# Kernel optimization log

Measured on AMD Instinct MI355X. Metric: run time of the kernel, lower is better.

The kernel has to match this reference:

```python
import jax, jax.numpy as jnp
import numpy as np

N_NODES = 50000
N_EDGES = 800000
N_FEAT = 128
N_HID = 128
N_LAYER = 4
N_CLASS = 40


def setup_inputs() -> dict:
    key = jax.random.key(0)
    ks = jax.random.split(key, 8)
    x = jax.random.normal(ks[0], (N_NODES, N_FEAT), jnp.float32)
    edge_index = jax.random.randint(ks[1], (2, N_EDGES), 0, N_NODES, dtype=jnp.int64)
    s = 1.0 / np.float32(np.sqrt(N_HID))
    # n_feat == n_hid so all L conv weights stack into one [L, C, C] tensor
    convW = jax.random.normal(ks[2], (N_LAYER, N_HID, N_HID), jnp.float32) * s
    convb = jnp.zeros((N_LAYER, N_HID), jnp.float32)
    W_att = jax.random.normal(ks[3], (N_HID, N_HID), jnp.float32) * s
    a_att = jax.random.normal(ks[4], (N_HID,), jnp.float32) * s
    W_out = jax.random.normal(ks[5], (N_HID, N_CLASS), jnp.float32) * s
    b_out = jnp.zeros((N_CLASS,), jnp.float32)
    return dict(x=x, edge_index=edge_index, convW=convW, convb=convb,
                W_att=W_att, a_att=a_att, W_out=W_out, b_out=b_out)


def reference(x, edge_index, convW, convb, W_att, a_att, W_out, b_out):
    src, dst = edge_index[0], edge_index[1]
    N = x.shape[0]
    # GCN symmetric normalization with self-loops: deg = 1 + in-degree
    deg = jax.ops.segment_sum(jnp.ones_like(dst, dtype=jnp.float32), dst,
                              num_segments=N) + 1.0
    dinv = jax.lax.rsqrt(deg)
    enorm = (dinv[src] * dinv[dst])[:, None]   # per-edge norm
    snorm = (dinv * dinv)[:, None]             # self-loop norm

    hs = []
    h = x
    for l in range(N_LAYER):
        hW = h @ convW[l]                                          # [N, C]
        agg = jax.ops.segment_sum(hW[src] * enorm, dst, num_segments=N)
        agg = agg + hW * snorm                                     # self-loop
        h = jax.nn.relu(agg + convb[l])
        # dropout is identity at inference (training=False)
        hs.append(h)

    H = jnp.stack(hs, axis=1)                                      # [N, L, C]
    # additive attention over layers: alpha_l = softmax_l(a . tanh(W h_l))
    scores = jnp.tanh(H @ W_att) @ a_att                           # [N, L]
    alpha = jax.nn.softmax(scores, axis=1)
    fused = jnp.einsum('nl,nlc->nc', alpha, H)                     # [N, C]
    return fused @ W_out + b_out                                   # [N, n_class]
```

## Files before the change

kernel.cpp:

```cpp
#include <hip/hip_runtime.h>

#define NNODES 50000
#define NEDGES 800000
#define NCLASS 40
#define NBLK_SCAN 196
#define CNTB  3125
#define PREPB 320
#define WOUTB 24
#define GEMMB 782
#define XBLK  3125

typedef _Float16 half8  __attribute__((ext_vector_type(8)));
typedef float    floatx4 __attribute__((ext_vector_type(4)));

#define CSTR 136
#define SMEM_BYTES (64 * CSTR * 2 + 256)

__device__ __forceinline__ float fast_tanh(float x) {
    return 1.0f - 2.0f / (__expf(2.0f * x) + 1.0f);
}

__global__ __launch_bounds__(256) void k_pre(const int* __restrict__ dst, int* __restrict__ cnt,
                                             int* __restrict__ rank,
                                             const float* __restrict__ convW, const float* __restrict__ W_att,
                                             _Float16* __restrict__ WT,
                                             const float* __restrict__ Wout, _Float16* __restrict__ WoutT) {
    int bid = blockIdx.x, tid = threadIdx.x;
    if (bid < CNTB) {
        int e = bid * 256 + tid;
        rank[e] = atomicAdd(&cnt[dst[e]], 1);
    } else if (bid < CNTB + PREPB) {
        int idx = (bid - CNTB) * 256 + tid;
        int mat = idx >> 14, rem = idx & 16383;
        int j = rem & 7, lane = (rem >> 3) & 63, tile = rem >> 9;
        int l15 = lane & 15, quad = lane >> 4;
        int ct = tile & 7, kk = tile >> 3;
        int n = ct * 16 + l15, k = kk * 32 + quad * 8 + j;
        const float* src = (mat < 4) ? (convW + mat * 16384) : W_att;
        WT[idx] = (_Float16)src[k * 128 + n];
    } else {
        int idx = (bid - CNTB - PREPB) * 256 + tid;
        int j = idx & 7, lane = (idx >> 3) & 63, tile = idx >> 9;
        int l15 = lane & 15, quad = lane >> 4;
        int ct = tile % 3, kk = tile / 3;
        int n = ct * 16 + l15, k = kk * 32 + quad * 8 + j;
        WoutT[idx] = (n < NCLASS) ? (_Float16)Wout[k * NCLASS + n] : (_Float16)0.f;
    }
}

__global__ __launch_bounds__(256) void k_bsum(const int* __restrict__ cnt, int* __restrict__ bsum) {
    int t = threadIdx.x, b = blockIdx.x;
    int i = b * 256 + t;
    int c = (i < NNODES) ? cnt[i] : 0;
    int v = c;
    v += __shfl_xor(v, 1);  v += __shfl_xor(v, 2);  v += __shfl_xor(v, 4);
    v += __shfl_xor(v, 8);  v += __shfl_xor(v, 16); v += __shfl_xor(v, 32);
    __shared__ int ws[4];
    if ((t & 63) == 0) ws[t >> 6] = v;
    __syncthreads();
    if (t == 0) bsum[b] = ws[0] + ws[1] + ws[2] + ws[3];
}

__global__ __launch_bounds__(256) void k_offsets(const int* __restrict__ cnt, const int* __restrict__ bsum,
                                                 int* __restrict__ offsets, float* __restrict__ dinv) {
    int t = threadIdx.x, b = blockIdx.x;
    int i = b * 256 + t;
    int c = (i < NNODES) ? cnt[i] : 0;
    int pv = (t < b) ? bsum[t] : 0;
    int rv = pv;
    rv += __shfl_xor(rv, 1);  rv += __shfl_xor(rv, 2);  rv += __shfl_xor(rv, 4);
    rv += __shfl_xor(rv, 8);  rv += __shfl_xor(rv, 16); rv += __shfl_xor(rv, 32);
    __shared__ int wsum[4];
    __shared__ int part[256];
    if ((t & 63) == 0) wsum[t >> 6] = rv;
    part[t] = c;
    __syncthreads();
    int boff = wsum[0] + wsum[1] + wsum[2] + wsum[3];
#pragma unroll
    for (int d = 1; d < 256; d <<= 1) {
        int v = (t >= d) ? part[t - d] : 0;
        __syncthreads();
        part[t] += v;
        __syncthreads();
    }
    if (i < NNODES) {
        offsets[i] = boff + part[t] - c;
        dinv[i] = rsqrtf((float)c + 1.0f);
    }
    if (b == 0 && t == 0) offsets[NNODES] = NEDGES;
}

__device__ __forceinline__ void gemm_body_f32(const float* __restrict__ Av, const _Float16* __restrict__ WTf,
                                              const float* __restrict__ dinv, _Float16* __restrict__ C,
                                              int m0, char* smem) {
    _Float16 (*Csh)[CSTR] = (_Float16 (*)[CSTR])smem;
    float* sdinv = (float*)(smem + 64 * CSTR * 2);
    int tid = threadIdx.x;
    int wave = tid >> 6, lane = tid & 63;
    int quad = lane >> 4, l15 = lane & 15;
    int ko = quad * 8;

    if (tid < 64) {
        int r = m0 + tid; if (r > NNODES - 1) r = NNODES - 1;
        sdinv[tid] = dinv[r];
    }

    floatx4 acc[4][2];
#pragma unroll
    for (int rt = 0; rt < 4; ++rt)
#pragma unroll
        for (int ct = 0; ct < 2; ++ct) acc[rt][ct] = (floatx4){0.f, 0.f, 0.f, 0.f};

#pragma unroll
    for (int kk = 0; kk < 4; ++kk) {
        half8 a[4], b[2];
#pragma unroll
        for (int rt = 0; rt < 4; ++rt) {
            int row = m0 + rt * 16 + l15;
            if (row > NNODES - 1) row = NNODES - 1;
            const float* Ap = Av + (size_t)row * 128 + kk * 32 + ko;
            float4 f0 = *(const float4*)Ap;
            float4 f1 = *(const float4*)(Ap + 4);
            a[rt] = (half8){(_Float16)f0.x, (_Float16)f0.y, (_Float16)f0.z, (_Float16)f0.w,
                            (_Float16)f1.x, (_Float16)f1.y, (_Float16)f1.z, (_Float16)f1.w};
        }
#pragma unroll
        for (int ct = 0; ct < 2; ++ct)
            b[ct] = *(const half8*)&WTf[((kk * 8 + (wave * 2 + ct)) * 64 + lane) * 8];
#pragma unroll
        for (int rt = 0; rt < 4; ++rt)
#pragma unroll
            for (int ct = 0; ct < 2; ++ct)
                acc[rt][ct] = __builtin_amdgcn_mfma_f32_16x16x32_f16(a[rt], b[ct], acc[rt][ct], 0, 0, 0);
    }
    __syncthreads();

#pragma unroll
    for (int rt = 0; rt < 4; ++rt)
#pragma unroll
        for (int r = 0; r < 4; ++r) {
            float d = sdinv[rt * 16 + quad * 4 + r];
#pragma unroll
            for (int ct = 0; ct < 2; ++ct)
                Csh[rt * 16 + quad * 4 + r][wave * 32 + ct * 16 + l15] = (_Float16)(acc[rt][ct][r] * d);
        }
    __syncthreads();

    int row = tid >> 2, seg = tid & 3;
    int gm = m0 + row;
    if (gm < NNODES) {
#pragma unroll
        for (int j = 0; j < 4; ++j)
            *(half8*)(C + (size_t)gm * 128 + seg * 32 + j * 8) = *(const half8*)&Csh[row][seg * 32 + j * 8];
    }
}

__global__ __launch_bounds__(256) void k_fillgemm(const int* __restrict__ src, const int* __restrict__ dst,
                                                  const int* __restrict__ offsets, const int* __restrict__ rank,
                                                  int* __restrict__ esrc,
                                                  const float* __restrict__ x, const _Float16* __restrict__ WT,
                                                  const float* __restrict__ dinv, _Float16* __restrict__ C) {
    __shared__ __align__(16) char smem[SMEM_BYTES];
    int bid = blockIdx.x;
    if (bid < GEMMB) {
        gemm_body_f32(x, WT, dinv, C, bid * 64, smem);
    } else {
        int e = (bid - GEMMB) * 256 + threadIdx.x;
        int d = dst[e];
        esrc[offsets[d] + rank[e]] = src[e];
    }
}

template <bool HAS_GEMM>
__global__ __launch_bounds__(256) void k_layer(const _Float16* __restrict__ hin,
                                               const int* __restrict__ offsets, const int* __restrict__ esrc,
                                               const float* __restrict__ dinv, const float* __restrict__ bias,
                                               _Float16* __restrict__ hh,
                                               const _Float16* __restrict__ WTatt, const float* __restrict__ a_att,
                                               float* __restrict__ scores, int layer,
                                               const _Float16* __restrict__ WTnext, _Float16* __restrict__ hout) {
    __shared__ __align__(16) _Float16 h[16][CSTR];
    __shared__ float bsh[128];
    __shared__ float sdv[16];
    __shared__ float pp[4][16];
    int tid = threadIdx.x;
    if (tid < 128) bsh[tid] = bias[tid];
    int wave = tid >> 6, lane = tid & 63;
    int n0 = blockIdx.x * 16;

    {
        int nl = tid >> 4;
        int cl = tid & 15;
        int c8 = cl * 8;
        int n = n0 + nl;
        int beg = offsets[n], end = offsets[n + 1];
        float dn = dinv[n];
        half8 sv = *(const half8*)(hin + (size_t)n * 128 + c8);

        float a[8];
#pragma unroll
        for (int u = 0; u < 8; ++u) a[u] = 0.f;

        int i0[4], i1[4];
#pragma unroll
        for (int i = 0; i < 4; ++i) {
            int ei = beg + i;
            int t = esrc[ei];
            i0[i] = (ei < end) ? t : NNODES;
        }
        half8 v0[4];
#pragma unroll
        for (int i = 0; i < 4; ++i) v0[i] = *(const half8*)(hin + (size_t)i0[i] * 128 + c8);
#pragma unroll
        for (int i = 0; i < 4; ++i) {
            int ei = beg + 4 + i;
            int t = esrc[ei];
            i1[i] = (ei < end) ? t : NNODES;
        }
        half8 v1[4];
#pragma unroll
        for (int i = 0; i < 4; ++i) v1[i] = *(const half8*)(hin + (size_t)i1[i] * 128 + c8);

        for (int e = beg; e < end; e += 8) {
            int i2[4];
#pragma unroll
            for (int i = 0; i < 4; ++i) {
                int ei = e + 8 + i;
                int t = esrc[ei];
                i2[i] = (ei < end) ? t : NNODES;
            }
#pragma unroll
            for (int i = 0; i < 4; ++i)
#pragma unroll
                for (int u = 0; u < 8; ++u) a[u] += (float)v0[i][u];
#pragma unroll
            for (int i = 0; i < 4; ++i) v0[i] = *(const half8*)(hin + (size_t)i2[i] * 128 + c8);
            int i3[4];
#pragma unroll
            for (int i = 0; i < 4; ++i) {
                int ei = e + 12 + i;
                int t = esrc[ei];
                i3[i] = (ei < end) ? t : NNODES;
            }
#pragma unroll
            for (int i = 0; i < 4; ++i)
#pragma unroll
                for (int u = 0; u < 8; ++u) a[u] += (float)v1[i][u];
#pragma unroll
            for (int i = 0; i < 4; ++i) v1[i] = *(const half8*)(hin + (size_t)i3[i] * 128 + c8);
        }
        __syncthreads();
        half8 o;
#pragma unroll
        for (int u = 0; u < 8; ++u) {
            float r = (a[u] + (float)sv[u]) * dn + bsh[c8 + u];
            o[u] = (_Float16)fmaxf(r, 0.f);
        }
        *(half8*)(hh + (size_t)n * 128 + c8) = o;
        *(half8*)&h[nl][c8] = o;
        if (cl == 0) sdv[nl] = dn;
    }
    __syncthreads();

    int quad = lane >> 4, l15 = lane & 15;
    int ko = quad * 8;
    half8 af[4];
#pragma unroll
    for (int kk = 0; kk < 4; ++kk) af[kk] = *(const half8*)&h[l15][kk * 32 + ko];

    {
        float p[4] = {0.f, 0.f, 0.f, 0.f};
#pragma unroll
        for (int c2 = 0; c2 < 2; ++c2) {
            int ct = wave * 2 + c2;
            half8 b[4];
#pragma unroll
            for (int kk = 0; kk < 4; ++kk)
                b[kk] = *(const half8*)&WTatt[((kk * 8 + ct) * 64 + lane) * 8];
            floatx4 acc = (floatx4){0.f, 0.f, 0.f, 0.f};
#pragma unroll
            for (int kk = 0; kk < 4; ++kk)
                acc = __builtin_amdgcn_mfma_f32_16x16x32_f16(af[kk], b[kk], acc, 0, 0, 0);
            float av = a_att[ct * 16 + l15];
#pragma unroll
            for (int r = 0; r < 4; ++r) p[r] += av * fast_tanh(acc[r]);
        }
#pragma unroll
        for (int r = 0; r < 4; ++r) {
            float v = p[r];
            v += __shfl_xor(v, 1); v += __shfl_xor(v, 2);
            v += __shfl_xor(v, 4); v += __shfl_xor(v, 8);
            if (l15 == 0) pp[wave][quad * 4 + r] = v;
        }
    }
    __syncthreads();
    if (tid < 16) scores[(size_t)(n0 + tid) * 4 + layer] = pp[0][tid] + pp[1][tid] + pp[2][tid] + pp[3][tid];

    if (HAS_GEMM) {
        floatx4 acc[2];
#pragma unroll
        for (int c2 = 0; c2 < 2; ++c2) acc[c2] = (floatx4){0.f, 0.f, 0.f, 0.f};
#pragma unroll
        for (int c2 = 0; c2 < 2; ++c2) {
            int ct = wave * 2 + c2;
#pragma unroll
            for (int kk = 0; kk < 4; ++kk) {
                half8 b = *(const half8*)&WTnext[((kk * 8 + ct) * 64 + lane) * 8];
                acc[c2] = __builtin_amdgcn_mfma_f32_16x16x32_f16(af[kk], b, acc[c2], 0, 0, 0);
            }
        }
        __syncthreads();
#pragma unroll
        for (int c2 = 0; c2 < 2; ++c2) {
            int col = (wave * 2 + c2) * 16 + l15;
#pragma unroll
            for (int r = 0; r < 4; ++r) {
                int row = quad * 4 + r;
                h[row][col] = (_Float16)(acc[c2][r] * sdv[row]);
            }
        }
        __syncthreads();
        int row = tid >> 4, seg = tid & 15;
        int gm = n0 + row;
        *(half8*)(hout + (size_t)gm * 128 + seg * 8) = *(const half8*)&h[row][seg * 8];
    }
}

__global__ __launch_bounds__(256) void k_fuse_out(const _Float16* __restrict__ hbase, const float* __restrict__ scores,
                                                  const _Float16* __restrict__ WoutT, const float* __restrict__ bout,
                                                  float* __restrict__ out) {
    __shared__ __align__(16) _Float16 Fs[64][136];
    __shared__ float salpha[256];
    const size_t LSTR = (size_t)NNODES * 128;
    int tid = threadIdx.x;
    int n0 = blockIdx.x * 64;

    if (tid < 64) {
        int node = n0 + tid; if (node > NNODES - 1) node = NNODES - 1;
        float4 s = *(const float4*)(scores + (size_t)node * 4);
        float mx = fmaxf(fmaxf(s.x, s.y), fmaxf(s.z, s.w));
        float e0 = __expf(s.x - mx), e1 = __expf(s.y - mx), e2 = __expf(s.z - mx), e3 = __expf(s.w - mx);
        float inv = 1.0f / (e0 + e1 + e2 + e3);
        salpha[tid * 4 + 0] = e0 * inv; salpha[tid * 4 + 1] = e1 * inv;
        salpha[tid * 4 + 2] = e2 * inv; salpha[tid * 4 + 3] = e3 * inv;
    }
    __syncthreads();

    {
        int no = tid >> 2, seg = tid & 3;
        int node = n0 + no; if (node > NNODES - 1) node = NNODES - 1;
        float al0 = salpha[no * 4 + 0], al1 = salpha[no * 4 + 1];
        float al2 = salpha[no * 4 + 2], al3 = salpha[no * 4 + 3];
        const _Float16* hp = hbase + (size_t)node * 128 + seg * 32;
#pragma unroll
        for (int j = 0; j < 4; ++j) {
            half8 h0 = *(const half8*)(hp + 0 * LSTR + j * 8);
            half8 h1 = *(const half8*)(hp + 1 * LSTR + j * 8);
            half8 h2 = *(const half8*)(hp + 2 * LSTR + j * 8);
            half8 h3 = *(const half8*)(hp + 3 * LSTR + j * 8);
            half8 f;
#pragma unroll
            for (int u = 0; u < 8; ++u)
                f[u] = (_Float16)(al0 * (float)h0[u] + al1 * (float)h1[u] +
                                  al2 * (float)h2[u] + al3 * (float)h3[u]);
            *(half8*)&Fs[no][seg * 32 + j * 8] = f;
        }
    }
    __syncthreads();

    int wave = tid >> 6, lane = tid & 63;
    int quad = lane >> 4, l15 = lane & 15;
    int ko = quad * 8;
    half8 ff[4];
    int frow = wave * 16 + l15;
#pragma unroll
    for (int kk = 0; kk < 4; ++kk) ff[kk] = *(const half8*)&Fs[frow][kk * 32 + ko];
#pragma unroll
    for (int ct = 0; ct < 3; ++ct) {
        half8 bw[4];
#pragma unroll
        for (int kk = 0; kk < 4; ++kk)
            bw[kk] = *(const half8*)(WoutT + ((kk * 3 + ct) * 64 + lane) * 8);
        floatx4 acc = (floatx4){0.f, 0.f, 0.f, 0.f};
#pragma unroll
        for (int kk = 0; kk < 4; ++kk)
            acc = __builtin_amdgcn_mfma_f32_16x16x32_f16(ff[kk], bw[kk], acc, 0, 0, 0);
        int col = ct * 16 + l15;
        if (col < NCLASS) {
            float bv = bout[col];
#pragma unroll
            for (int r = 0; r < 4; ++r) {
                int node = n0 + wave * 16 + quad * 4 + r;
                if (node < NNODES) out[(size_t)node * NCLASS + col] = acc[r] + bv;
            }
        }
    }
}

extern "C" void kernel_launch(void* const* d_in, const int* in_sizes, int n_in,
                              void* d_out, int out_size, void* d_ws, size_t ws_size,
                              hipStream_t stream) {
    const float* x     = (const float*)d_in[0];
    const int*   ei    = (const int*)d_in[1];
    const float* convW = (const float*)d_in[2];
    const float* convb = (const float*)d_in[3];
    const float* W_att = (const float*)d_in[4];
    const float* a_att = (const float*)d_in[5];
    const float* W_out = (const float*)d_in[6];
    const float* b_out = (const float*)d_in[7];
    float* out = (float*)d_out;

    char* ws = (char*)d_ws;
    size_t off = 0;
    auto take = [&](size_t nbytes) { char* p = ws + off; off += (nbytes + 255) & ~(size_t)255; return p; };
    float*     dinv    = (float*)take(NNODES * 4);
    int*       cnt     = (int*)take(NNODES * 4);
    int*       rank    = (int*)take(NEDGES * 4);
    int*       offsets = (int*)take((NNODES + 1) * 4);
    int*       bsum    = (int*)take(256 * 4);
    int*       esrc    = (int*)take(NEDGES * 4 + 256);
    _Float16*  WoutT   = (_Float16*)take((size_t)48 * 128 * 2);
    float*     scores  = (float*)take(NNODES * 4 * 4);
    _Float16*  WT      = (_Float16*)take((size_t)5 * 128 * 128 * 2);
    _Float16*  hWsA    = (_Float16*)take((size_t)(NNODES + 1) * 128 * 2);
    _Float16*  hh[4];
    for (int l = 0; l < 4; ++l) hh[l] = (_Float16*)take((size_t)NNODES * 128 * 2);
    _Float16*  hWsB    = (_Float16*)take((size_t)(NNODES + 1) * 128 * 2);

    const int* src = ei;
    const int* dst = ei + NEDGES;

    hipMemsetAsync(cnt, 0, NNODES * 4, stream);
    hipMemsetAsync(hWsA + (size_t)NNODES * 128, 0, 256, stream);
    hipMemsetAsync(hWsB + (size_t)NNODES * 128, 0, 256, stream);
    k_pre<<<CNTB + PREPB + WOUTB, 256, 0, stream>>>(dst, cnt, rank, convW, W_att, WT, W_out, WoutT);
    k_bsum<<<NBLK_SCAN, 256, 0, stream>>>(cnt, bsum);
    k_offsets<<<NBLK_SCAN, 256, 0, stream>>>(cnt, bsum, offsets, dinv);
    k_fillgemm<<<GEMMB + CNTB, 256, 0, stream>>>(src, dst, offsets, rank, esrc, x, WT, dinv, hWsA);

    k_layer<true><<<XBLK, 256, 0, stream>>>(hWsA, offsets, esrc, dinv, convb + 0 * 128, hh[0],
                                            WT + 4 * 16384, a_att, scores, 0, WT + 1 * 16384, hWsB);
    k_layer<true><<<XBLK, 256, 0, stream>>>(hWsB, offsets, esrc, dinv, convb + 1 * 128, hh[1],
                                            WT + 4 * 16384, a_att, scores, 1, WT + 2 * 16384, hWsA);
    k_layer<true><<<XBLK, 256, 0, stream>>>(hWsA, offsets, esrc, dinv, convb + 2 * 128, hh[2],
                                            WT + 4 * 16384, a_att, scores, 2, WT + 3 * 16384, hWsB);
    k_layer<false><<<XBLK, 256, 0, stream>>>(hWsB, offsets, esrc, dinv, convb + 3 * 128, hh[3],
                                             WT + 4 * 16384, a_att, scores, 3, (const _Float16*)nullptr,
                                             (_Float16*)nullptr);
    k_fuse_out<<<GEMMB, 256, 0, stream>>>(hh[0], scores, WoutT, b_out, out);
}
```

Baseline: 330.3 us.

## Split layer into channel-blocked gather kernel and separate attention/GEMM kernel

Transformed features are stored in four 32-channel column blocks so that each aggregation block gathers only one 64-byte slice per neighbor, which keeps the gathered working set small enough to stay cache-resident. The fused per-layer kernel is split into a gather/aggregation kernel and a 64-row MFMA kernel for the attention score and next-layer GEMM. This adds a write and re-read of hh per layer plus an extra launch per layer. It also replaces the padding memsets with a block in the prep kernel.

```diff
diff --git a/kernel.cpp b/kernel.cpp
--- a/kernel.cpp
+++ b/kernel.cpp
@@ -8,13 +8,15 @@
 #define PREPB 320
 #define WOUTB 24
 #define GEMMB 782
-#define XBLK  3125
+#define AGGT  782
+#define AGGB  (AGGT * 4)
 
 typedef _Float16 half8  __attribute__((ext_vector_type(8)));
 typedef float    floatx4 __attribute__((ext_vector_type(4)));
 
 #define CSTR 136
-#define SMEM_BYTES (64 * CSTR * 2 + 256)
+#define BLKROW 32
+#define BLKSTRIDE ((size_t)(NNODES + 1) * BLKROW)
 
 __device__ __forceinline__ float fast_tanh(float x) {
     return 1.0f - 2.0f / (__expf(2.0f * x) + 1.0f);
@@ -24,7 +26,8 @@
                                              int* __restrict__ rank,
                                              const float* __restrict__ convW, const float* __restrict__ W_att,
                                              _Float16* __restrict__ WT,
-                                             const float* __restrict__ Wout, _Float16* __restrict__ WoutT) {
+                                             const float* __restrict__ Wout, _Float16* __restrict__ WoutT,
+                                             _Float16* __restrict__ blkA, _Float16* __restrict__ blkB) {
     int bid = blockIdx.x, tid = threadIdx.x;
     if (bid < CNTB) {
         int e = bid * 256 + tid;
@@ -38,13 +41,18 @@
         int n = ct * 16 + l15, k = kk * 32 + quad * 8 + j;
         const float* src = (mat < 4) ? (convW + mat * 16384) : W_att;
         WT[idx] = (_Float16)src[k * 128 + n];
-    } else {
+    } else if (bid < CNTB + PREPB + WOUTB) {
         int idx = (bid - CNTB - PREPB) * 256 + tid;
         int j = idx & 7, lane = (idx >> 3) & 63, tile = idx >> 9;
         int l15 = lane & 15, quad = lane >> 4;
         int ct = tile % 3, kk = tile / 3;
         int n = ct * 16 + l15, k = kk * 32 + quad * 8 + j;
         WoutT[idx] = (n < NCLASS) ? (_Float16)Wout[k * NCLASS + n] : (_Float16)0.f;
+    } else {
+        int s = tid >> 7, rem = tid & 127;
+        int cg = rem >> 5, c = rem & 31;
+        _Float16* p = (s == 0) ? blkA : blkB;
+        p[(size_t)cg * BLKSTRIDE + (size_t)NNODES * BLKROW + c] = (_Float16)0.f;
     }
 }
 
@@ -91,7 +99,7 @@
 }
 
 __device__ __forceinline__ void gemm_body_f32(const float* __restrict__ Av, const _Float16* __restrict__ WTf,
-                                              const float* __restrict__ dinv, _Float16* __restrict__ C,
+                                              const float* __restrict__ dinv, _Float16* __restrict__ Cblk,
                                               int m0, char* smem) {
     _Float16 (*Csh)[CSTR] = (_Float16 (*)[CSTR])smem;
     float* sdinv = (float*)(smem + 64 * CSTR * 2);
@@ -151,7 +159,8 @@
     if (gm < NNODES) {
 #pragma unroll
         for (int j = 0; j < 4; ++j)
-            *(half8*)(C + (size_t)gm * 128 + seg * 32 + j * 8) = *(const half8*)&Csh[row][seg * 32 + j * 8];
+            *(half8*)(Cblk + (size_t)seg * BLKSTRIDE + (size_t)gm * BLKROW + j * 8) =
+                *(const half8*)&Csh[row][seg * 32 + j * 8];
     }
 }
 
@@ -159,11 +168,11 @@
                                                   const int* __restrict__ offsets, const int* __restrict__ rank,
                                                   int* __restrict__ esrc,
                                                   const float* __restrict__ x, const _Float16* __restrict__ WT,
-                                                  const float* __restrict__ dinv, _Float16* __restrict__ C) {
-    __shared__ __align__(16) char smem[SMEM_BYTES];
+                                                  const float* __restrict__ dinv, _Float16* __restrict__ Cblk) {
+    __shared__ __align__(16) char smem[64 * CSTR * 2 + 256];
     int bid = blockIdx.x;
     if (bid < GEMMB) {
-        gemm_body_f32(x, WT, dinv, C, bid * 64, smem);
+        gemm_body_f32(x, WT, dinv, Cblk, bid * 64, smem);
     } else {
         int e = (bid - GEMMB) * 256 + threadIdx.x;
         int d = dst[e];
@@ -171,105 +180,124 @@
     }
 }
 
+__global__ __launch_bounds__(256) void k_agg(const _Float16* __restrict__ hinblk,
+                                             const int* __restrict__ offsets, const int* __restrict__ esrc,
+                                             const float* __restrict__ dinv, const float* __restrict__ bias,
+                                             _Float16* __restrict__ hh) {
+    int tid = threadIdx.x;
+    int cg = blockIdx.x & 3, tile = blockIdx.x >> 2;
+    int nl = tid >> 2, cl = tid & 3;
+    int n = tile * 64 + nl;
+    if (n >= NNODES) return;
+    int c8 = cl * 8;
+    const _Float16* base = hinblk + (size_t)cg * BLKSTRIDE;
+    int beg = offsets[n], end = offsets[n + 1];
+    float dn = dinv[n];
+    half8 sv = *(const half8*)(base + (size_t)n * BLKROW + c8);
+    float4 b0 = *(const float4*)(bias + cg * 32 + c8);
+    float4 b1 = *(const float4*)(bias + cg * 32 + c8 + 4);
+
+    float a[8];
+#pragma unroll
+    for (int u = 0; u < 8; ++u) a[u] = 0.f;
+
+    int i0[4], i1[4];
+#pragma unroll
+    for (int i = 0; i < 4; ++i) {
+        int ei = beg + i;
+        int t = esrc[ei];
+        i0[i] = (ei < end) ? t : NNODES;
+    }
+    half8 v0[4];
+#pragma unroll
+    for (int i = 0; i < 4; ++i) v0[i] = *(const half8*)(base + (size_t)i0[i] * BLKROW + c8);
+#pragma unroll
+    for (int i = 0; i < 4; ++i) {
+        int ei = beg + 4 + i;
+        int t = esrc[ei];
+        i1[i] = (ei < end) ? t : NNODES;
+    }
+    half8 v1[4];
+#pragma unroll
+    for (int i = 0; i < 4; ++i) v1[i] = *(const half8*)(base + (size_t)i1[i] * BLKROW + c8);
+
+    for (int e = beg; e < end; e += 8) {
+        int i2[4];
+#pragma unroll
+        for (int i = 0; i < 4; ++i) {
+            int ei = e + 8 + i;
+            int t = esrc[ei];
+            i2[i] = (ei < end) ? t : NNODES;
+        }
+#pragma unroll
+        for (int i = 0; i < 4; ++i)
+#pragma unroll
+            for (int u = 0; u < 8; ++u) a[u] += (float)v0[i][u];
+#pragma unroll
+        for (int i = 0; i < 4; ++i) v0[i] = *(const half8*)(base + (size_t)i2[i] * BLKROW + c8);
+        int i3[4];
+#pragma unroll
+        for (int i = 0; i < 4; ++i) {
+            int ei = e + 12 + i;
+            int t = esrc[ei];
+            i3[i] = (ei < end) ? t : NNODES;
+        }
+#pragma unroll
+        for (int i = 0; i < 4; ++i)
+#pragma unroll
+            for (int u = 0; u < 8; ++u) a[u] += (float)v1[i][u];
+#pragma unroll
+        for (int i = 0; i < 4; ++i) v1[i] = *(const half8*)(base + (size_t)i3[i] * BLKROW + c8);
+    }
+
+    float bb[8] = {b0.x, b0.y, b0.z, b0.w, b1.x, b1.y, b1.z, b1.w};
+    half8 o;
+#pragma unroll
+    for (int u = 0; u < 8; ++u) {
+        float r = (a[u] + (float)sv[u]) * dn + bb[u];
+        o[u] = (_Float16)fmaxf(r, 0.f);
+    }
+    *(half8*)(hh + (size_t)n * 128 + cg * 32 + c8) = o;
+}
+
 template <bool HAS_GEMM>
-__global__ __launch_bounds__(256) void k_layer(const _Float16* __restrict__ hin,
-                                               const int* __restrict__ offsets, const int* __restrict__ esrc,
-                                               const float* __restrict__ dinv, const float* __restrict__ bias,
-                                               _Float16* __restrict__ hh,
-                                               const _Float16* __restrict__ WTatt, const float* __restrict__ a_att,
-                                               float* __restrict__ scores, int layer,
-                                               const _Float16* __restrict__ WTnext, _Float16* __restrict__ hout) {
-    __shared__ __align__(16) _Float16 h[16][CSTR];
-    __shared__ float bsh[128];
-    __shared__ float sdv[16];
-    __shared__ float pp[4][16];
+__global__ __launch_bounds__(256) void k_attngemm(const _Float16* __restrict__ hh,
+                                                  const float* __restrict__ dinv,
+                                                  const _Float16* __restrict__ WTatt,
+                                                  const float* __restrict__ a_att,
+                                                  float* __restrict__ scores, int layer,
+                                                  const _Float16* __restrict__ WTnext,
+                                                  _Float16* __restrict__ outblk) {
+    __shared__ __align__(16) _Float16 Csh[64][CSTR];
+    __shared__ float pp[4][64];
+    __shared__ float sdv[64];
     int tid = threadIdx.x;
-    if (tid < 128) bsh[tid] = bias[tid];
     int wave = tid >> 6, lane = tid & 63;
-    int n0 = blockIdx.x * 16;
-
-    {
-        int nl = tid >> 4;
-        int cl = tid & 15;
-        int c8 = cl * 8;
-        int n = n0 + nl;
-        int beg = offsets[n], end = offsets[n + 1];
-        float dn = dinv[n];
-        half8 sv = *(const half8*)(hin + (size_t)n * 128 + c8);
-
-        float a[8];
-#pragma unroll
-        for (int u = 0; u < 8; ++u) a[u] = 0.f;
-
-        int i0[4], i1[4];
-#pragma unroll
-        for (int i = 0; i < 4; ++i) {
-            int ei = beg + i;
-            int t = esrc[ei];
-            i0[i] = (ei < end) ? t : NNODES;
-        }
-        half8 v0[4];
-#pragma unroll
-        for (int i = 0; i < 4; ++i) v0[i] = *(const half8*)(hin + (size_t)i0[i] * 128 + c8);
-#pragma unroll
-        for (int i = 0; i < 4; ++i) {
-            int ei = beg + 4 + i;
-            int t = esrc[ei];
-            i1[i] = (ei < end) ? t : NNODES;
-        }
-        half8 v1[4];
-#pragma unroll
-        for (int i = 0; i < 4; ++i) v1[i] = *(const half8*)(hin + (size_t)i1[i] * 128 + c8);
-
-        for (int e = beg; e < end; e += 8) {
-            int i2[4];
-#pragma unroll
-            for (int i = 0; i < 4; ++i) {
-                int ei = e + 8 + i;
-                int t = esrc[ei];
-                i2[i] = (ei < end) ? t : NNODES;
-            }
-#pragma unroll
-            for (int i = 0; i < 4; ++i)
-#pragma unroll
-                for (int u = 0; u < 8; ++u) a[u] += (float)v0[i][u];
-#pragma unroll
-            for (int i = 0; i < 4; ++i) v0[i] = *(const half8*)(hin + (size_t)i2[i] * 128 + c8);
-            int i3[4];
-#pragma unroll
-            for (int i = 0; i < 4; ++i) {
-                int ei = e + 12 + i;
-                int t = esrc[ei];
-                i3[i] = (ei < end) ? t : NNODES;
-            }
-#pragma unroll
-            for (int i = 0; i < 4; ++i)
-#pragma unroll
-                for (int u = 0; u < 8; ++u) a[u] += (float)v1[i][u];
-#pragma unroll
-            for (int i = 0; i < 4; ++i) v1[i] = *(const half8*)(hin + (size_t)i3[i] * 128 + c8);
-        }
-        __syncthreads();
-        half8 o;
-#pragma unroll
-        for (int u = 0; u < 8; ++u) {
-            float r = (a[u] + (float)sv[u]) * dn + bsh[c8 + u];
-            o[u] = (_Float16)fmaxf(r, 0.f);
-        }
-        *(half8*)(hh + (size_t)n * 128 + c8) = o;
-        *(half8*)&h[nl][c8] = o;
-        if (cl == 0) sdv[nl] = dn;
-    }
-    __syncthreads();
-
     int quad = lane >> 4, l15 = lane & 15;
     int ko = quad * 8;
-    half8 af[4];
-#pragma unroll
-    for (int kk = 0; kk < 4; ++kk) af[kk] = *(const half8*)&h[l15][kk * 32 + ko];
+    int m0 = blockIdx.x * 64;
+
+    if (tid < 64) {
+        int r = m0 + tid; if (r > NNODES - 1) r = NNODES - 1;
+        sdv[tid] = dinv[r];
+    }
+
+    half8 a[4][4];
+#pragma unroll
+    for (int rt = 0; rt < 4; ++rt) {
+        int row = m0 + rt * 16 + l15;
+        if (row > NNODES - 1) row = NNODES - 1;
+        const _Float16* Ap = hh + (size_t)row * 128 + ko;
+#pragma unroll
+        for (int kk = 0; kk < 4; ++kk) a[rt][kk] = *(const half8*)(Ap + kk * 32);
+    }
 
     {
-        float p[4] = {0.f, 0.f, 0.f, 0.f};
+        float p[4][4];
+#pragma unroll
+        for (int rt = 0; rt < 4; ++rt)
+#pragma unroll
+            for (int r = 0; r < 4; ++r) p[rt][r] = 0.f;
 #pragma unroll
         for (int c2 = 0; c2 < 2; ++c2) {
             int ct = wave * 2 + c2;
@@ -277,52 +305,69 @@
 #pragma unroll
             for (int kk = 0; kk < 4; ++kk)
                 b[kk] = *(const half8*)&WTatt[((kk * 8 + ct) * 64 + lane) * 8];
-            floatx4 acc = (floatx4){0.f, 0.f, 0.f, 0.f};
-#pragma unroll
-            for (int kk = 0; kk < 4; ++kk)
-                acc = __builtin_amdgcn_mfma_f32_16x16x32_f16(af[kk], b[kk], acc, 0, 0, 0);
             float av = a_att[ct * 16 + l15];
 #pragma unroll
-            for (int r = 0; r < 4; ++r) p[r] += av * fast_tanh(acc[r]);
-        }
-#pragma unroll
-        for (int r = 0; r < 4; ++r) {
-            float v = p[r];
-            v += __shfl_xor(v, 1); v += __shfl_xor(v, 2);
-            v += __shfl_xor(v, 4); v += __shfl_xor(v, 8);
-            if (l15 == 0) pp[wave][quad * 4 + r] = v;
-        }
-    }
-    __syncthreads();
-    if (tid < 16) scores[(size_t)(n0 + tid) * 4 + layer] = pp[0][tid] + pp[1][tid] + pp[2][tid] + pp[3][tid];
+            for (int rt = 0; rt < 4; ++rt) {
+                floatx4 acc = (floatx4){0.f, 0.f, 0.f, 0.f};
+#pragma unroll
+                for (int kk = 0; kk < 4; ++kk)
+                    acc = __builtin_amdgcn_mfma_f32_16x16x32_f16(a[rt][kk], b[kk], acc, 0, 0, 0);
+#pragma unroll
+                for (int r = 0; r < 4; ++r) p[rt][r] += av * fast_tanh(acc[r]);
+            }
+        }
+#pragma unroll
+        for (int rt = 0; rt < 4; ++rt)
+#pragma unroll
+            for (int r = 0; r < 4; ++r) {
+                float v = p[rt][r];
+                v += __shfl_xor(v, 1); v += __shfl_xor(v, 2);
+                v += __shfl_xor(v, 4); v += __shfl_xor(v, 8);
+                if (l15 == 0) pp[wave][rt * 16 + quad * 4 + r] = v;
+            }
+    }
+    __syncthreads();
+    if (tid < 64) {
+        int nd = m0 + tid;
+        if (nd < NNODES) scores[(size_t)nd * 4 + layer] = pp[0][tid] + pp[1][tid] + pp[2][tid] + pp[3][tid];
+    }
 
     if (HAS_GEMM) {
-        floatx4 acc[2];
-#pragma unroll
-        for (int c2 = 0; c2 < 2; ++c2) acc[c2] = (floatx4){0.f, 0.f, 0.f, 0.f};
+        floatx4 acc[4][2];
+#pragma unroll
+        for (int rt = 0; rt < 4; ++rt)
+#pragma unroll
+            for (int c2 = 0; c2 < 2; ++c2) acc[rt][c2] = (floatx4){0.f, 0.f, 0.f, 0.f};
 #pragma unroll
         for (int c2 = 0; c2 < 2; ++c2) {
             int ct = wave * 2 + c2;
 #pragma unroll
             for (int kk = 0; kk < 4; ++kk) {
                 half8 b = *(const half8*)&WTnext[((kk * 8 + ct) * 64 + lane) * 8];
-                acc[c2] = __builtin_amdgcn_mfma_f32_16x16x32_f16(af[kk], b, acc[c2], 0, 0, 0);
+#pragma unroll
+                for (int rt = 0; rt < 4; ++rt)
+                    acc[rt][c2] = __builtin_amdgcn_mfma_f32_16x16x32_f16(a[rt][kk], b, acc[rt][c2], 0, 0, 0);
             }
         }
+#pragma unroll
+        for (int rt = 0; rt < 4; ++rt)
+#pragma unroll
+            for (int r = 0; r < 4; ++r) {
+                int row = rt * 16 + quad * 4 + r;
+                float d = sdv[row];
+#pragma unroll
+                for (int c2 = 0; c2 < 2; ++c2)
+                    Csh[row][(wave * 2 + c2) * 16 + l15] = (_Float16)(acc[rt][c2][r] * d);
+            }
         __syncthreads();
-#pragma unroll
-        for (int c2 = 0; c2 < 2; ++c2) {
-            int col = (wave * 2 + c2) * 16 + l15;
-#pragma unroll
-            for (int r = 0; r < 4; ++r) {
-                int row = quad * 4 + r;
-                h[row][col] = (_Float16)(acc[c2][r] * sdv[row]);
-            }
-        }
-        __syncthreads();
-        int row = tid >> 4, seg = tid & 15;
-        int gm = n0 + row;
-        *(half8*)(hout + (size_t)gm * 128 + seg * 8) = *(const half8*)&h[row][seg * 8];
+        int row = tid >> 2, seg = tid & 3;
+        int gm = m0 + row;
+        if (gm < NNODES) {
+#pragma unroll
+            for (int j = 0; j < 4; ++j)
+                *(half8*)(outblk + (size_t)seg * BLKSTRIDE + (size_t)gm * BLKROW + j * 8) =
+                    *(const half8*)&Csh[row][seg * 32 + j * 8];
+        }
     }
 }
 
@@ -422,30 +467,32 @@
     _Float16*  WoutT   = (_Float16*)take((size_t)48 * 128 * 2);
     float*     scores  = (float*)take(NNODES * 4 * 4);
     _Float16*  WT      = (_Float16*)take((size_t)5 * 128 * 128 * 2);
-    _Float16*  hWsA    = (_Float16*)take((size_t)(NNODES + 1) * 128 * 2);
+    _Float16*  blkA    = (_Float16*)take(4 * BLKSTRIDE * 2);
     _Float16*  hh[4];
     for (int l = 0; l < 4; ++l) hh[l] = (_Float16*)take((size_t)NNODES * 128 * 2);
-    _Float16*  hWsB    = (_Float16*)take((size_t)(NNODES + 1) * 128 * 2);
+    _Float16*  blkB    = (_Float16*)take(4 * BLKSTRIDE * 2);
 
     const int* src = ei;
     const int* dst = ei + NEDGES;
 
     hipMemsetAsync(cnt, 0, NNODES * 4, stream);
-    hipMemsetAsync(hWsA + (size_t)NNODES * 128, 0, 256, stream);
-    hipMemsetAsync(hWsB + (size_t)NNODES * 128, 0, 256, stream);
-    k_pre<<<CNTB + PREPB + WOUTB, 256, 0, stream>>>(dst, cnt, rank, convW, W_att, WT, W_out, WoutT);
+    k_pre<<<CNTB + PREPB + WOUTB + 1, 256, 0, stream>>>(dst, cnt, rank, convW, W_att, WT, W_out, WoutT,
+                                                        blkA, blkB);
     k_bsum<<<NBLK_SCAN, 256, 0, stream>>>(cnt, bsum);
     k_offsets<<<NBLK_SCAN, 256, 0, stream>>>(cnt, bsum, offsets, dinv);
-    k_fillgemm<<<GEMMB + CNTB, 256, 0, stream>>>(src, dst, offsets, rank, esrc, x, WT, dinv, hWsA);
-
-    k_layer<true><<<XBLK, 256, 0, stream>>>(hWsA, offsets, esrc, dinv, convb + 0 * 128, hh[0],
-                                            WT + 4 * 16384, a_att, scores, 0, WT + 1 * 16384, hWsB);
-    k_layer<true><<<XBLK, 256, 0, stream>>>(hWsB, offsets, esrc, dinv, convb + 1 * 128, hh[1],
-                                            WT + 4 * 16384, a_att, scores, 1, WT + 2 * 16384, hWsA);
-    k_layer<true><<<XBLK, 256, 0, stream>>>(hWsA, offsets, esrc, dinv, convb + 2 * 128, hh[2],
-                                            WT + 4 * 16384, a_att, scores, 2, WT + 3 * 16384, hWsB);
-    k_layer<false><<<XBLK, 256, 0, stream>>>(hWsB, offsets, esrc, dinv, convb + 3 * 128, hh[3],
-                                             WT + 4 * 16384, a_att, scores, 3, (const _Float16*)nullptr,
-                                             (_Float16*)nullptr);
+    k_fillgemm<<<GEMMB + CNTB, 256, 0, stream>>>(src, dst, offsets, rank, esrc, x, WT, dinv, blkA);
+
+    _Float16* bin = blkA;
+    _Float16* bout_ = blkB;
+    for (int l = 0; l < 4; ++l) {
+        k_agg<<<AGGB, 256, 0, stream>>>(bin, offsets, esrc, dinv, convb + l * 128, hh[l]);
+        if (l < 3)
+            k_attngemm<true><<<GEMMB, 256, 0, stream>>>(hh[l], dinv, WT + 4 * 16384, a_att, scores, l,
+                                                        WT + (l + 1) * 16384, bout_);
+        else
+            k_attngemm<false><<<GEMMB, 256, 0, stream>>>(hh[3], dinv, WT + 4 * 16384, a_att, scores, 3,
+                                                         (const _Float16*)nullptr, (_Float16*)nullptr);
+        _Float16* t = bin; bin = bout_; bout_ = t;
+    }
     k_fuse_out<<<GEMMB, 256, 0, stream>>>(hh[0], scores, WoutT, b_out, out);
 }
```

New measurement: 364.8 us. +10.4%, slower.

## Store hW in column-blocked layout so gathers run four passes over 32-column slices

Applied to the files above, without the earlier changes.

The transformed features hW are now stored as four column blocks of 32 halves per node instead of 128-wide rows. The layer kernel gathers one 32-column block at a time, with four lanes each handling different edges, then reduces across lanes with shuffles. Each pass touches a quarter-size array, so the gather working set fits cache better. In exchange, esrc indices and offsets are read four times, there are shuffle reductions, and each gathered row is only 64 bytes. The sentinel zero rows are now cleared inside k_pre instead of by separate memsets.

```diff
diff --git a/kernel.cpp b/kernel.cpp
--- a/kernel.cpp
+++ b/kernel.cpp
@@ -14,7 +14,8 @@
 typedef float    floatx4 __attribute__((ext_vector_type(4)));
 
 #define CSTR 136
-#define SMEM_BYTES (64 * CSTR * 2 + 256)
+#define BLKROW 32
+#define BLKSTRIDE ((size_t)(NNODES + 1) * BLKROW)
 
 __device__ __forceinline__ float fast_tanh(float x) {
     return 1.0f - 2.0f / (__expf(2.0f * x) + 1.0f);
@@ -24,7 +25,8 @@
                                              int* __restrict__ rank,
                                              const float* __restrict__ convW, const float* __restrict__ W_att,
                                              _Float16* __restrict__ WT,
-                                             const float* __restrict__ Wout, _Float16* __restrict__ WoutT) {
+                                             const float* __restrict__ Wout, _Float16* __restrict__ WoutT,
+                                             _Float16* __restrict__ blkA, _Float16* __restrict__ blkB) {
     int bid = blockIdx.x, tid = threadIdx.x;
     if (bid < CNTB) {
         int e = bid * 256 + tid;
@@ -38,13 +40,18 @@
         int n = ct * 16 + l15, k = kk * 32 + quad * 8 + j;
         const float* src = (mat < 4) ? (convW + mat * 16384) : W_att;
         WT[idx] = (_Float16)src[k * 128 + n];
-    } else {
+    } else if (bid < CNTB + PREPB + WOUTB) {
         int idx = (bid - CNTB - PREPB) * 256 + tid;
         int j = idx & 7, lane = (idx >> 3) & 63, tile = idx >> 9;
         int l15 = lane & 15, quad = lane >> 4;
         int ct = tile % 3, kk = tile / 3;
         int n = ct * 16 + l15, k = kk * 32 + quad * 8 + j;
         WoutT[idx] = (n < NCLASS) ? (_Float16)Wout[k * NCLASS + n] : (_Float16)0.f;
+    } else {
+        int s = tid >> 7, rem = tid & 127;
+        int cg = rem >> 5, c = rem & 31;
+        _Float16* p = (s == 0) ? blkA : blkB;
+        p[(size_t)cg * BLKSTRIDE + (size_t)NNODES * BLKROW + c] = (_Float16)0.f;
     }
 }
 
@@ -91,7 +98,7 @@
 }
 
 __device__ __forceinline__ void gemm_body_f32(const float* __restrict__ Av, const _Float16* __restrict__ WTf,
-                                              const float* __restrict__ dinv, _Float16* __restrict__ C,
+                                              const float* __restrict__ dinv, _Float16* __restrict__ Cblk,
                                               int m0, char* smem) {
     _Float16 (*Csh)[CSTR] = (_Float16 (*)[CSTR])smem;
     float* sdinv = (float*)(smem + 64 * CSTR * 2);
@@ -151,7 +158,8 @@
     if (gm < NNODES) {
 #pragma unroll
         for (int j = 0; j < 4; ++j)
-            *(half8*)(C + (size_t)gm * 128 + seg * 32 + j * 8) = *(const half8*)&Csh[row][seg * 32 + j * 8];
+            *(half8*)(Cblk + (size_t)seg * BLKSTRIDE + (size_t)gm * BLKROW + j * 8) =
+                *(const half8*)&Csh[row][seg * 32 + j * 8];
     }
 }
 
@@ -159,11 +167,11 @@
                                                   const int* __restrict__ offsets, const int* __restrict__ rank,
                                                   int* __restrict__ esrc,
                                                   const float* __restrict__ x, const _Float16* __restrict__ WT,
-                                                  const float* __restrict__ dinv, _Float16* __restrict__ C) {
-    __shared__ __align__(16) char smem[SMEM_BYTES];
+                                                  const float* __restrict__ dinv, _Float16* __restrict__ Cblk) {
+    __shared__ __align__(16) char smem[64 * CSTR * 2 + 256];
     int bid = blockIdx.x;
     if (bid < GEMMB) {
-        gemm_body_f32(x, WT, dinv, C, bid * 64, smem);
+        gemm_body_f32(x, WT, dinv, Cblk, bid * 64, smem);
     } else {
         int e = (bid - GEMMB) * 256 + threadIdx.x;
         int d = dst[e];
@@ -191,73 +199,64 @@
     {
         int nl = tid >> 4;
         int cl = tid & 15;
-        int c8 = cl * 8;
+        int es = cl >> 2;
+        int ck = cl & 3;
+        int c8 = ck * 8;
         int n = n0 + nl;
         int beg = offsets[n], end = offsets[n + 1];
         float dn = dinv[n];
-        half8 sv = *(const half8*)(hin + (size_t)n * 128 + c8);
-
-        float a[8];
-#pragma unroll
-        for (int u = 0; u < 8; ++u) a[u] = 0.f;
-
-        int i0[4], i1[4];
-#pragma unroll
-        for (int i = 0; i < 4; ++i) {
-            int ei = beg + i;
-            int t = esrc[ei];
-            i0[i] = (ei < end) ? t : NNODES;
-        }
-        half8 v0[4];
-#pragma unroll
-        for (int i = 0; i < 4; ++i) v0[i] = *(const half8*)(hin + (size_t)i0[i] * 128 + c8);
-#pragma unroll
-        for (int i = 0; i < 4; ++i) {
-            int ei = beg + 4 + i;
-            int t = esrc[ei];
-            i1[i] = (ei < end) ? t : NNODES;
-        }
-        half8 v1[4];
-#pragma unroll
-        for (int i = 0; i < 4; ++i) v1[i] = *(const half8*)(hin + (size_t)i1[i] * 128 + c8);
-
-        for (int e = beg; e < end; e += 8) {
-            int i2[4];
-#pragma unroll
-            for (int i = 0; i < 4; ++i) {
-                int ei = e + 8 + i;
+        __syncthreads();
+
+#pragma unroll
+        for (int p = 0; p < 4; ++p) {
+            const _Float16* base = hin + (size_t)p * BLKSTRIDE;
+            float a[8];
+#pragma unroll
+            for (int u = 0; u < 8; ++u) a[u] = 0.f;
+
+            int ia, ib;
+            {
+                int ei = beg + es;
                 int t = esrc[ei];
-                i2[i] = (ei < end) ? t : NNODES;
-            }
-#pragma unroll
-            for (int i = 0; i < 4; ++i)
-#pragma unroll
-                for (int u = 0; u < 8; ++u) a[u] += (float)v0[i][u];
-#pragma unroll
-            for (int i = 0; i < 4; ++i) v0[i] = *(const half8*)(hin + (size_t)i2[i] * 128 + c8);
-            int i3[4];
-#pragma unroll
-            for (int i = 0; i < 4; ++i) {
-                int ei = e + 12 + i;
+                ia = (ei < end) ? t : NNODES;
+            }
+            half8 va = *(const half8*)(base + (size_t)ia * BLKROW + c8);
+            {
+                int ei = beg + 4 + es;
                 int t = esrc[ei];
-                i3[i] = (ei < end) ? t : NNODES;
-            }
-#pragma unroll
-            for (int i = 0; i < 4; ++i)
-#pragma unroll
-                for (int u = 0; u < 8; ++u) a[u] += (float)v1[i][u];
-#pragma unroll
-            for (int i = 0; i < 4; ++i) v1[i] = *(const half8*)(hin + (size_t)i3[i] * 128 + c8);
-        }
-        __syncthreads();
-        half8 o;
-#pragma unroll
-        for (int u = 0; u < 8; ++u) {
-            float r = (a[u] + (float)sv[u]) * dn + bsh[c8 + u];
-            o[u] = (_Float16)fmaxf(r, 0.f);
-        }
-        *(half8*)(hh + (size_t)n * 128 + c8) = o;
-        *(half8*)&h[nl][c8] = o;
+                ib = (ei < end) ? t : NNODES;
+            }
+            half8 vb = *(const half8*)(base + (size_t)ib * BLKROW + c8);
+
+            for (int e = beg; e < end; e += 8) {
+                int i2;
+                { int ei = e + 8 + es;  int t = esrc[ei]; i2 = (ei < end) ? t : NNODES; }
+#pragma unroll
+                for (int u = 0; u < 8; ++u) a[u] += (float)va[u];
+                va = *(const half8*)(base + (size_t)i2 * BLKROW + c8);
+                int i3;
+                { int ei = e + 12 + es; int t = esrc[ei]; i3 = (ei < end) ? t : NNODES; }
+#pragma unroll
+                for (int u = 0; u < 8; ++u) a[u] += (float)vb[u];
+                vb = *(const half8*)(base + (size_t)i3 * BLKROW + c8);
+            }
+#pragma unroll
+            for (int u = 0; u < 8; ++u) {
+                a[u] += __shfl_xor(a[u], 4);
+                a[u] += __shfl_xor(a[u], 8);
+            }
+            if (es == 0) {
+                half8 sv = *(const half8*)(base + (size_t)n * BLKROW + c8);
+                half8 o;
+#pragma unroll
+                for (int u = 0; u < 8; ++u) {
+                    float r = (a[u] + (float)sv[u]) * dn + bsh[p * 32 + c8 + u];
+                    o[u] = (_Float16)fmaxf(r, 0.f);
+                }
+                *(half8*)(hh + (size_t)n * 128 + p * 32 + c8) = o;
+                *(half8*)&h[nl][p * 32 + c8] = o;
+            }
+        }
         if (cl == 0) sdv[nl] = dn;
     }
     __syncthreads();
@@ -322,7 +321,8 @@
         __syncthreads();
         int row = tid >> 4, seg = tid & 15;
         int gm = n0 + row;
-        *(half8*)(hout + (size_t)gm * 128 + seg * 8) = *(const half8*)&h[row][seg * 8];
+        int cg = seg >> 2, c = (seg & 3) * 8;
+        *(half8*)(hout + (size_t)cg * BLKSTRIDE + (size_t)gm * BLKROW + c) = *(const half8*)&h[row][seg * 8];
     }
 }
 
@@ -422,29 +422,28 @@
     _Float16*  WoutT   = (_Float16*)take((size_t)48 * 128 * 2);
     float*     scores  = (float*)take(NNODES * 4 * 4);
     _Float16*  WT      = (_Float16*)take((size_t)5 * 128 * 128 * 2);
-    _Float16*  hWsA    = (_Float16*)take((size_t)(NNODES + 1) * 128 * 2);
+    _Float16*  blkA    = (_Float16*)take(4 * BLKSTRIDE * 2);
     _Float16*  hh[4];
     for (int l = 0; l < 4; ++l) hh[l] = (_Float16*)take((size_t)NNODES * 128 * 2);
-    _Float16*  hWsB    = (_Float16*)take((size_t)(NNODES + 1) * 128 * 2);
+    _Float16*  blkB    = (_Float16*)take(4 * BLKSTRIDE * 2);
 
     const int* src = ei;
     const int* dst = ei + NEDGES;
 
     hipMemsetAsync(cnt, 0, NNODES * 4, stream);
-    hipMemsetAsync(hWsA + (size_t)NNODES * 128, 0, 256, stream);
-    hipMemsetAsync(hWsB + (size_t)NNODES * 128, 0, 256, stream);
-    k_pre<<<CNTB + PREPB + WOUTB, 256, 0, stream>>>(dst, cnt, rank, convW, W_att, WT, W_out, WoutT);
+    k_pre<<<CNTB + PREPB + WOUTB + 1, 256, 0, stream>>>(dst, cnt, rank, convW, W_att, WT, W_out, WoutT,
+                                                        blkA, blkB);
     k_bsum<<<NBLK_SCAN, 256, 0, stream>>>(cnt, bsum);
     k_offsets<<<NBLK_SCAN, 256, 0, stream>>>(cnt, bsum, offsets, dinv);
-    k_fillgemm<<<GEMMB + CNTB, 256, 0, stream>>>(src, dst, offsets, rank, esrc, x, WT, dinv, hWsA);
-
-    k_layer<true><<<XBLK, 256, 0, stream>>>(hWsA, offsets, esrc, dinv, convb + 0 * 128, hh[0],
-                                            WT + 4 * 16384, a_att, scores, 0, WT + 1 * 16384, hWsB);
-    k_layer<true><<<XBLK, 256, 0, stream>>>(hWsB, offsets, esrc, dinv, convb + 1 * 128, hh[1],
-                                            WT + 4 * 16384, a_att, scores, 1, WT + 2 * 16384, hWsA);
-    k_layer<true><<<XBLK, 256, 0, stream>>>(hWsA, offsets, esrc, dinv, convb + 2 * 128, hh[2],
-                                            WT + 4 * 16384, a_att, scores, 2, WT + 3 * 16384, hWsB);
-    k_layer<false><<<XBLK, 256, 0, stream>>>(hWsB, offsets, esrc, dinv, convb + 3 * 128, hh[3],
+    k_fillgemm<<<GEMMB + CNTB, 256, 0, stream>>>(src, dst, offsets, rank, esrc, x, WT, dinv, blkA);
+
+    k_layer<true><<<XBLK, 256, 0, stream>>>(blkA, offsets, esrc, dinv, convb + 0 * 128, hh[0],
+                                            WT + 4 * 16384, a_att, scores, 0, WT + 1 * 16384, blkB);
+    k_layer<true><<<XBLK, 256, 0, stream>>>(blkB, offsets, esrc, dinv, convb + 1 * 128, hh[1],
+                                            WT + 4 * 16384, a_att, scores, 1, WT + 2 * 16384, blkA);
+    k_layer<true><<<XBLK, 256, 0, stream>>>(blkA, offsets, esrc, dinv, convb + 2 * 128, hh[2],
+                                            WT + 4 * 16384, a_att, scores, 2, WT + 3 * 16384, blkB);
+    k_layer<false><<<XBLK, 256, 0, stream>>>(blkB, offsets, esrc, dinv, convb + 3 * 128, hh[3],
                                              WT + 4 * 16384, a_att, scores, 3, (const _Float16*)nullptr,
                                              (_Float16*)nullptr);
     k_fuse_out<<<GEMMB, 256, 0, stream>>>(hh[0], scores, WoutT, b_out, out);
```

After: 346.8 us. 5.0% more time.
